# Performance work log

Measured on AMD Instinct MI355X. Metric: run time of the kernel, lower is better.

## Reference

```python
import jax, jax.numpy as jnp
import numpy as np

N = 50000
IN_DIM, HID, LAT = 128, 256, 64
E = 800000


def setup_inputs() -> dict:
    key = jax.random.key(0)
    ks = jax.random.split(key, 12)
    x = jax.random.normal(ks[0], (N, IN_DIM), dtype=jnp.float32)
    edge_index = jax.random.randint(ks[1], (2, E), 0, N, dtype=jnp.int64)
    edge_weight = jax.random.uniform(ks[2], (E,), dtype=jnp.float32)
    def w(k, i, o):
        return jax.random.normal(k, (i, o), dtype=jnp.float32) * 0.05
    return {
        "x": x, "edge_index": edge_index, "edge_weight": edge_weight,
        "W1": w(ks[3], IN_DIM, HID), "b1": jnp.zeros((HID,), jnp.float32),
        "W2": w(ks[4], HID, LAT),    "b2": jnp.zeros((LAT,), jnp.float32),
        "W3": w(ks[5], LAT, HID),    "b3": jnp.zeros((HID,), jnp.float32),
        "W4": w(ks[6], HID, IN_DIM), "b4": jnp.zeros((IN_DIM,), jnp.float32),
    }


def _gcn_norm(edge_index, edge_weight, n):
    # add self loops with weight 1 (PyG GCNConv default), symmetric normalization
    loop = jnp.arange(n, dtype=edge_index.dtype)
    row = jnp.concatenate([edge_index[0], loop])
    col = jnp.concatenate([edge_index[1], loop])
    ew = jnp.concatenate([edge_weight, jnp.ones((n,), edge_weight.dtype)])
    deg = jax.ops.segment_sum(ew, col, num_segments=n)  # [N]
    dinv = jnp.where(deg > 0, jax.lax.rsqrt(deg), 0.0)
    norm = dinv[row] * ew * dinv[col]                   # [E+N]
    return row, col, norm


def _gcn_conv(x, row, col, norm, W, b, n):
    h = x @ W                                           # [N, out]
    msg = h[row] * norm[:, None]                        # gather + scale [E+N, out]
    out = jax.ops.segment_sum(msg, col, num_segments=n) # scatter-add
    return out + b


def reference(x, edge_index, edge_weight, W1, b1, W2, b2, W3, b3, W4, b4):
    n = x.shape[0]
    row, col, norm = _gcn_norm(edge_index, edge_weight, n)
    # encode (dropout is identity in eval mode)
    h = jax.nn.relu(_gcn_conv(x, row, col, norm, W1, b1, n))
    z = _gcn_conv(h, row, col, norm, W2, b2, n)
    # decode
    h = jax.nn.relu(_gcn_conv(z, row, col, norm, W3, b3, n))
    x_recon = _gcn_conv(h, row, col, norm, W4, b4, n)
    return x_recon
```

## Files before the change

### kernel.cpp

```cpp
#include <hip/hip_runtime.h>
#include <hip/hip_fp16.h>

#define IN_DIM 128
#define HID    256
#define LAT    64

typedef __attribute__((ext_vector_type(8))) short bf16x8;
typedef __attribute__((ext_vector_type(4))) float f32x4;

__device__ __forceinline__ short f2bf(float f) {
    union { float f; unsigned u; } v; v.f = f;
    unsigned r = v.u + 0x7fffu + ((v.u >> 16) & 1u);
    return (short)(r >> 16);
}
__device__ __forceinline__ float bf2f(short s) {
    union { unsigned u; float f; } v; v.u = ((unsigned)(unsigned short)s) << 16;
    return v.f;
}

__device__ __forceinline__ void storeP(__half* p, float v) { *p = __float2half(v); }
__device__ __forceinline__ void storeP(float*  p, float v) { *p = v; }


#define FIXSCALE 1048576.0f

__global__ void k_init(unsigned long long* __restrict__ packed, int n) {
    int i = blockIdx.x * 256 + threadIdx.x;
    if (i < n) packed[i] = (unsigned long long)(1u << 20);
}

__global__ void k_edge_acc(const int* __restrict__ ei, const float* __restrict__ ew,
                           unsigned long long* __restrict__ packed,
                           int* __restrict__ rank, int E) {
    int e = blockIdx.x * 256 + threadIdx.x;
    if (e < E) {
        int c = ei[E + e];
        unsigned fx = (unsigned)lrintf(ew[e] * FIXSCALE);
        unsigned long long old =
            atomicAdd(&packed[c], ((unsigned long long)1 << 40) | (unsigned long long)fx);
        rank[e] = (int)(old >> 40);
    }
}

__global__ void k_derive(const unsigned long long* __restrict__ packed,
                         float* __restrict__ dinv, int* __restrict__ counts, int n) {
    int i = blockIdx.x * 256 + threadIdx.x;
    if (i < n) {
        unsigned long long p = packed[i];
        float deg = (float)(p & (((unsigned long long)1 << 40) - 1)) * (1.0f / FIXSCALE);
        dinv[i]   = rsqrtf(deg);
        counts[i] = (int)(p >> 40);
    }
}

__global__ __launch_bounds__(1024) void k_blocksum(const int* __restrict__ counts,
                                                   int* __restrict__ bsum, int n) {
    __shared__ int ws[16];
    const int t = threadIdx.x, lane = t & 63, wv = t >> 6;
    int i = blockIdx.x * 1024 + t;
    int v = (i < n) ? counts[i] : 0;
    #pragma unroll
    for (int d = 1; d < 64; d <<= 1) v += __shfl_xor(v, d);
    if (lane == 0) ws[wv] = v;
    __syncthreads();
    if (wv == 0 && lane < 16) {
        int x = ws[lane];
        #pragma unroll
        for (int d = 1; d < 16; d <<= 1) x += __shfl_xor(x, d, 16);
        if (lane == 0) bsum[blockIdx.x] = x;
    }
}

__global__ void k_scan_bsums(int* __restrict__ bsum, int nb,
                             int* __restrict__ offsets, int n) {
    int lane = threadIdx.x;
    int v = (lane < nb) ? bsum[lane] : 0;
    #pragma unroll
    for (int d = 1; d < 64; d <<= 1) {
        int u = __shfl_up(v, d);
        if (lane >= d) v += u;
    }
    if (lane < nb) bsum[lane] = v;
    if (lane == nb - 1) offsets[n] = v;
}

__global__ __launch_bounds__(1024) void k_scan_apply(const int* __restrict__ counts,
                                                     const int* __restrict__ bsum,
                                                     int* __restrict__ offsets, int n) {
    __shared__ int ws[16];
    const int t = threadIdx.x, lane = t & 63, wv = t >> 6;
    int i = blockIdx.x * 1024 + t;
    int v = (i < n) ? counts[i] : 0;
    int s = v;
    #pragma unroll
    for (int d = 1; d < 64; d <<= 1) {
        int u = __shfl_up(s, d);
        if (lane >= d) s += u;
    }
    if (lane == 63) ws[wv] = s;
    __syncthreads();
    if (wv == 0 && lane < 16) {
        int x = ws[lane];
        #pragma unroll
        for (int d = 1; d < 16; d <<= 1) {
            int u = __shfl_up(x, d, 16);
            if (lane >= d) x += u;
        }
        ws[lane] = x;
    }
    __syncthreads();
    int base = (blockIdx.x ? bsum[blockIdx.x - 1] : 0) + (wv ? ws[wv - 1] : 0);
    if (i < n) offsets[i] = base + s - v;
}

__global__ void k_fill(const int* __restrict__ ei, const float* __restrict__ ew,
                       const float* __restrict__ dinv, const int* __restrict__ offsets,
                       const int* __restrict__ rank,
                       int* __restrict__ csr_row, float* __restrict__ csr_norm, int E) {
    int e = blockIdx.x * 256 + threadIdx.x;
    if (e < E) {
        int r = ei[e];
        int c = ei[E + e];
        int pos = offsets[c] + rank[e];
        csr_row[pos]  = r;
        csr_norm[pos] = dinv[r] * ew[e] * dinv[c];
    }
}

template <int BN, typename PT>
__global__ __launch_bounds__(256) void gemm_mfma(const float* __restrict__ A,
                                                 const float* __restrict__ W,
                                                 PT* __restrict__ P,
                                                 int M, int K, int F) {
    constexpr int WC = BN / 32;
    __shared__ alignas(16) short Ahi[128][40];
    __shared__ alignas(16) short Alo[128][40];
    __shared__ alignas(16) short Whi[BN][40];
    __shared__ alignas(16) short Wlo[BN][40];

    const int bm  = blockIdx.x * 128;
    const int bn  = blockIdx.y * BN;
    const int tid = threadIdx.x;
    const int wv  = tid >> 6;
    const int wy  = wv >> 1;
    const int wx  = wv & 1;
    const int lane = tid & 63;
    const int frow = lane & 15;
    const int fk   = (lane >> 4) * 8;

    const int wc_ = tid % BN;
    const int kg  = tid / BN;
    constexpr int KC = 32 * BN / 256;

    f32x4 acc[4][WC];
    #pragma unroll
    for (int i = 0; i < 4; ++i)
        #pragma unroll
        for (int j = 0; j < WC; ++j)
            acc[i][j] = (f32x4){0.f, 0.f, 0.f, 0.f};

    for (int k0 = 0; k0 < K; k0 += 32) {
        if (k0) __syncthreads();
        #pragma unroll
        for (int it = 0; it < 4; ++it) {
            int l   = tid + it * 256;
            int row = l >> 3;
            int k4  = l & 7;
            int gr  = bm + row;
            float4 v = make_float4(0.f, 0.f, 0.f, 0.f);
            if (gr < M) v = *(const float4*)&A[(size_t)gr * K + k0 + k4 * 4];
            float vv[4] = {v.x, v.y, v.z, v.w};
            short h[4], lo[4];
            #pragma unroll
            for (int j = 0; j < 4; ++j) {
                h[j]  = f2bf(vv[j]);
                lo[j] = f2bf(vv[j] - bf2f(h[j]));
            }
            *(short4*)&Ahi[row][k4 * 4] = make_short4(h[0], h[1], h[2], h[3]);
            *(short4*)&Alo[row][k4 * 4] = make_short4(lo[0], lo[1], lo[2], lo[3]);
        }
        #pragma unroll
        for (int kk = 0; kk < KC; kk += 4) {
            short h[4], lo[4];
            #pragma unroll
            for (int j = 0; j < 4; ++j) {
                float w = W[(size_t)(k0 + kg * KC + kk + j) * F + bn + wc_];
                h[j]  = f2bf(w);
                lo[j] = f2bf(w - bf2f(h[j]));
            }
            *(short4*)&Whi[wc_][kg * KC + kk] = make_short4(h[0], h[1], h[2], h[3]);
            *(short4*)&Wlo[wc_][kg * KC + kk] = make_short4(lo[0], lo[1], lo[2], lo[3]);
        }
        __syncthreads();
        bf16x8 ah[4], al[4], wh[WC], wl[WC];
        #pragma unroll
        for (int ar = 0; ar < 4; ++ar) {
            ah[ar] = *(const bf16x8*)&Ahi[wy * 64 + ar * 16 + frow][fk];
            al[ar] = *(const bf16x8*)&Alo[wy * 64 + ar * 16 + frow][fk];
        }
        #pragma unroll
        for (int wc = 0; wc < WC; ++wc) {
            wh[wc] = *(const bf16x8*)&Whi[wx * (BN / 2) + wc * 16 + frow][fk];
            wl[wc] = *(const bf16x8*)&Wlo[wx * (BN / 2) + wc * 16 + frow][fk];
        }
        #pragma unroll
        for (int ar = 0; ar < 4; ++ar)
            #pragma unroll
            for (int wc = 0; wc < WC; ++wc) {
                acc[ar][wc] = __builtin_amdgcn_mfma_f32_16x16x32_bf16(ah[ar], wh[wc], acc[ar][wc], 0, 0, 0);
                acc[ar][wc] = __builtin_amdgcn_mfma_f32_16x16x32_bf16(ah[ar], wl[wc], acc[ar][wc], 0, 0, 0);
                acc[ar][wc] = __builtin_amdgcn_mfma_f32_16x16x32_bf16(al[ar], wh[wc], acc[ar][wc], 0, 0, 0);
            }
    }
    #pragma unroll
    for (int ar = 0; ar < 4; ++ar)
        #pragma unroll
        for (int r = 0; r < 4; ++r) {
            int row = bm + wy * 64 + ar * 16 + (lane >> 4) * 4 + r;
            if (row >= M) continue;
            #pragma unroll
            for (int wc = 0; wc < WC; ++wc) {
                int col = bn + wx * (BN / 2) + wc * 16 + (lane & 15);
                storeP(&P[(size_t)row * F + col], acc[ar][wc][r]);
            }
        }
}


template <int VEC>
__device__ __forceinline__ void pload(float* d, const __half* s) {
    if constexpr (VEC == 4) {
        union { short4 s4; __half h[4]; } u;
        u.s4 = *(const short4*)s;
        #pragma unroll
        for (int j = 0; j < 4; ++j) d[j] = __half2float(u.h[j]);
    } else if constexpr (VEC == 2) {
        union { short2 s2; __half h[2]; } u;
        u.s2 = *(const short2*)s;
        d[0] = __half2float(u.h[0]); d[1] = __half2float(u.h[1]);
    } else {
        d[0] = __half2float(*s);
    }
}
template <int VEC>
__device__ __forceinline__ void pload(float* d, const float* s) {
    if constexpr (VEC == 4) { float4 v = *(const float4*)s; d[0]=v.x; d[1]=v.y; d[2]=v.z; d[3]=v.w; }
    else if constexpr (VEC == 2) { float2 v = *(const float2*)s; d[0]=v.x; d[1]=v.y; }
    else { d[0] = *s; }
}
template <int VEC>
__device__ __forceinline__ void fstore(float* d, const float* s) {
    if constexpr (VEC == 4) { *(float4*)d = make_float4(s[0], s[1], s[2], s[3]); }
    else if constexpr (VEC == 2) { *(float2*)d = make_float2(s[0], s[1]); }
    else { *d = s[0]; }
}

template <int VEC, bool RELU, typename PT>
__global__ __launch_bounds__(256) void agg_kernel(
    const PT* __restrict__ pre, const float* __restrict__ bias,
    const int* __restrict__ offsets, const int* __restrict__ csr_row,
    const float* __restrict__ csr_norm, const float* __restrict__ dinv,
    float* __restrict__ out, int n) {
    constexpr int F = VEC * 64;
    const int wave = threadIdx.x >> 6;
    const int lane = threadIdx.x & 63;
    const int c = blockIdx.x * 4 + wave;
    if (c >= n) return;
    const float di = dinv[c];
    const float sn = di * di;
    float acc[VEC], t0[VEC], t1[VEC], t2[VEC], t3[VEC], bv[VEC];
    pload<VEC>(acc, pre + (size_t)c * F + lane * VEC);
    #pragma unroll
    for (int v = 0; v < VEC; ++v) acc[v] *= sn;
    const int beg = offsets[c], end = offsets[c + 1];
    int j = beg;
    for (; j + 3 < end; j += 4) {
        int   r0 = csr_row[j],      r1 = csr_row[j + 1];
        int   r2 = csr_row[j + 2],  r3 = csr_row[j + 3];
        float w0 = csr_norm[j],     w1 = csr_norm[j + 1];
        float w2 = csr_norm[j + 2], w3 = csr_norm[j + 3];
        pload<VEC>(t0, pre + (size_t)r0 * F + lane * VEC);
        pload<VEC>(t1, pre + (size_t)r1 * F + lane * VEC);
        pload<VEC>(t2, pre + (size_t)r2 * F + lane * VEC);
        pload<VEC>(t3, pre + (size_t)r3 * F + lane * VEC);
        #pragma unroll
        for (int v = 0; v < VEC; ++v) acc[v] = fmaf(w0, t0[v], acc[v]);
        #pragma unroll
        for (int v = 0; v < VEC; ++v) acc[v] = fmaf(w1, t1[v], acc[v]);
        #pragma unroll
        for (int v = 0; v < VEC; ++v) acc[v] = fmaf(w2, t2[v], acc[v]);
        #pragma unroll
        for (int v = 0; v < VEC; ++v) acc[v] = fmaf(w3, t3[v], acc[v]);
    }
    for (; j < end; ++j) {
        int r0 = csr_row[j]; float w0 = csr_norm[j];
        pload<VEC>(t0, pre + (size_t)r0 * F + lane * VEC);
        #pragma unroll
        for (int v = 0; v < VEC; ++v) acc[v] = fmaf(w0, t0[v], acc[v]);
    }
    pload<VEC>(bv, bias + lane * VEC);
    #pragma unroll
    for (int v = 0; v < VEC; ++v) {
        float o = acc[v] + bv[v];
        if (RELU) o = fmaxf(o, 0.f);
        acc[v] = o;
    }
    fstore<VEC>(out + (size_t)c * F + lane * VEC, acc);
}


extern "C" void kernel_launch(void* const* d_in, const int* in_sizes, int n_in,
                              void* d_out, int out_size, void* d_ws, size_t ws_size,
                              hipStream_t stream) {
    const float* x  = (const float*)d_in[0];
    const int*   ei = (const int*)  d_in[1];
    const float* ew = (const float*)d_in[2];
    const float* W1 = (const float*)d_in[3];
    const float* b1 = (const float*)d_in[4];
    const float* W2 = (const float*)d_in[5];
    const float* b2 = (const float*)d_in[6];
    const float* W3 = (const float*)d_in[7];
    const float* b3 = (const float*)d_in[8];
    const float* W4 = (const float*)d_in[9];
    const float* b4 = (const float*)d_in[10];

    const int N = in_sizes[0] / IN_DIM;
    const int E = in_sizes[2];

    char* p = (char*)d_ws;
    auto alloc = [&](size_t bytes) -> void* {
        void* r = (void*)p;
        p += (bytes + 255) & ~(size_t)255;
        return r;
    };
    unsigned long long* packed = (unsigned long long*)alloc((size_t)N * 8);
    float*  dinv     = (float*)alloc((size_t)N * 4);
    int*    counts   = (int*)  alloc((size_t)N * 4);
    int*    offsets  = (int*)  alloc((size_t)(N + 1) * 4);
    int*    bsum     = (int*)  alloc((size_t)64 * 4);
    int*    rank     = (int*)  alloc((size_t)E * 4);
    int*    csr_row  = (int*)  alloc((size_t)E * 4);
    float*  csr_norm = (float*)alloc((size_t)E * 4);
    __half* bufP     = (__half*)alloc((size_t)N * HID * 2);
    float*  bufH     = (float*) alloc((size_t)N * HID * 4);
    float*  bufZ     = (float*) alloc((size_t)N * LAT * 4);
    float*  bufP32   = (float*)bufP;

    const int gN  = (N + 255) / 256;
    const int gE  = (E + 255) / 256;
    const int nbS = (N + 1023) / 1024;
    const int nbM = (N + 127) / 128;
    const int nodeBlocks = (N + 3) / 4;

    k_init      <<<gN, 256, 0, stream>>>(packed, N);
    k_edge_acc  <<<gE, 256, 0, stream>>>(ei, ew, packed, rank, E);
    k_derive    <<<gN, 256, 0, stream>>>(packed, dinv, counts, N);
    k_blocksum  <<<nbS, 1024, 0, stream>>>(counts, bsum, N);
    k_scan_bsums<<<1, 64, 0, stream>>>(bsum, nbS, offsets, N);
    k_scan_apply<<<nbS, 1024, 0, stream>>>(counts, bsum, offsets, N);
    k_fill      <<<gE, 256, 0, stream>>>(ei, ew, dinv, offsets, rank, csr_row, csr_norm, E);

    gemm_mfma<128, __half><<<dim3(nbM, HID / 128), 256, 0, stream>>>(x, W1, bufP, N, IN_DIM, HID);
    agg_kernel<4, true, __half><<<nodeBlocks, 256, 0, stream>>>(bufP, b1, offsets, csr_row, csr_norm, dinv, bufH, N);

    gemm_mfma<64, __half><<<dim3(nbM, LAT / 64), 256, 0, stream>>>(bufH, W2, bufP, N, HID, LAT);
    agg_kernel<1, false, __half><<<nodeBlocks, 256, 0, stream>>>(bufP, b2, offsets, csr_row, csr_norm, dinv, bufZ, N);

    gemm_mfma<128, __half><<<dim3(nbM, HID / 128), 256, 0, stream>>>(bufZ, W3, bufP, N, LAT, HID);
    agg_kernel<4, true, __half><<<nodeBlocks, 256, 0, stream>>>(bufP, b3, offsets, csr_row, csr_norm, dinv, bufH, N);

    gemm_mfma<128, float><<<dim3(nbM, IN_DIM / 128), 256, 0, stream>>>(bufH, W4, bufP32, N, HID, IN_DIM);
    agg_kernel<2, false, float><<<nodeBlocks, 256, 0, stream>>>(bufP32, b4, offsets, csr_row, csr_norm, dinv, (float*)d_out, N);
}
```

Baseline: 480.9 us.

## Reorder GCN layers to aggregate at narrower width and fuse bias+ReLU into GEMM

For layers 1 and 3, the aggregation now runs before the matrix multiply, using associativity (A·X)·W. The gather therefore runs at 128 or 64 features instead of 256, and the bias+ReLU is applied in the GEMM epilogue. Edge row indices and norms are packed into one int2 CSR array so each edge needs a single load, and the input x is cast to fp16 first to halve gather traffic. The cost is an extra cast kernel and fp16 rounding of x and z, which could change accuracy.

```diff
diff --git a/kernel.cpp b/kernel.cpp
--- a/kernel.cpp
+++ b/kernel.cpp
@@ -116,20 +116,35 @@
 __global__ void k_fill(const int* __restrict__ ei, const float* __restrict__ ew,
                        const float* __restrict__ dinv, const int* __restrict__ offsets,
                        const int* __restrict__ rank,
-                       int* __restrict__ csr_row, float* __restrict__ csr_norm, int E) {
+                       int2* __restrict__ csr, int E) {
     int e = blockIdx.x * 256 + threadIdx.x;
     if (e < E) {
         int r = ei[e];
         int c = ei[E + e];
         int pos = offsets[c] + rank[e];
-        csr_row[pos]  = r;
-        csr_norm[pos] = dinv[r] * ew[e] * dinv[c];
-    }
-}
-
-template <int BN, typename PT>
+        float nm = dinv[r] * ew[e] * dinv[c];
+        csr[pos] = make_int2(r, __float_as_int(nm));
+    }
+}
+
+__global__ void k_cast(const float* __restrict__ x, __half* __restrict__ xh, int total) {
+    int idx = (blockIdx.x * 256 + threadIdx.x) * 8;
+    if (idx < total) {
+        float4 a = *(const float4*)&x[idx];
+        float4 b = *(const float4*)&x[idx + 4];
+        short4 s0 = make_short4(__half_as_short(__float2half(a.x)), __half_as_short(__float2half(a.y)),
+                                __half_as_short(__float2half(a.z)), __half_as_short(__float2half(a.w)));
+        short4 s1 = make_short4(__half_as_short(__float2half(b.x)), __half_as_short(__float2half(b.y)),
+                                __half_as_short(__float2half(b.z)), __half_as_short(__float2half(b.w)));
+        *(short4*)&xh[idx]     = s0;
+        *(short4*)&xh[idx + 4] = s1;
+    }
+}
+
+template <int BN, typename PT, bool EPI>
 __global__ __launch_bounds__(256) void gemm_mfma(const float* __restrict__ A,
                                                  const float* __restrict__ W,
+                                                 const float* __restrict__ bias,
                                                  PT* __restrict__ P,
                                                  int M, int K, int F) {
     constexpr int WC = BN / 32;
@@ -221,7 +236,9 @@
             #pragma unroll
             for (int wc = 0; wc < WC; ++wc) {
                 int col = bn + wx * (BN / 2) + wc * 16 + (lane & 15);
-                storeP(&P[(size_t)row * F + col], acc[ar][wc][r]);
+                float o = acc[ar][wc][r];
+                if (EPI) o = fmaxf(o + bias[col], 0.f);
+                storeP(&P[(size_t)row * F + col], o);
             }
         }
 }
@@ -249,18 +266,28 @@
     else { d[0] = *s; }
 }
 template <int VEC>
-__device__ __forceinline__ void fstore(float* d, const float* s) {
+__device__ __forceinline__ void pstore(__half* d, const float* s) {
+    if constexpr (VEC == 4) {
+        *(short4*)d = make_short4(__half_as_short(__float2half(s[0])), __half_as_short(__float2half(s[1])),
+                                  __half_as_short(__float2half(s[2])), __half_as_short(__float2half(s[3])));
+    } else if constexpr (VEC == 2) {
+        *(short2*)d = make_short2(__half_as_short(__float2half(s[0])), __half_as_short(__float2half(s[1])));
+    } else {
+        *d = __float2half(s[0]);
+    }
+}
+template <int VEC>
+__device__ __forceinline__ void pstore(float* d, const float* s) {
     if constexpr (VEC == 4) { *(float4*)d = make_float4(s[0], s[1], s[2], s[3]); }
     else if constexpr (VEC == 2) { *(float2*)d = make_float2(s[0], s[1]); }
     else { *d = s[0]; }
 }
 
-template <int VEC, bool RELU, typename PT>
+template <int VEC, bool HASB, typename TIN, typename TOUT>
 __global__ __launch_bounds__(256) void agg_kernel(
-    const PT* __restrict__ pre, const float* __restrict__ bias,
-    const int* __restrict__ offsets, const int* __restrict__ csr_row,
-    const float* __restrict__ csr_norm, const float* __restrict__ dinv,
-    float* __restrict__ out, int n) {
+    const TIN* __restrict__ pre, const float* __restrict__ bias,
+    const int* __restrict__ offsets, const int2* __restrict__ csr,
+    const float* __restrict__ dinv, TOUT* __restrict__ out, int n) {
     constexpr int F = VEC * 64;
     const int wave = threadIdx.x >> 6;
     const int lane = threadIdx.x & 63;
@@ -268,44 +295,41 @@
     if (c >= n) return;
     const float di = dinv[c];
     const float sn = di * di;
-    float acc[VEC], t0[VEC], t1[VEC], t2[VEC], t3[VEC], bv[VEC];
+    float acc[VEC], t0[VEC], t1[VEC], t2[VEC], t3[VEC];
     pload<VEC>(acc, pre + (size_t)c * F + lane * VEC);
     #pragma unroll
     for (int v = 0; v < VEC; ++v) acc[v] *= sn;
     const int beg = offsets[c], end = offsets[c + 1];
     int j = beg;
     for (; j + 3 < end; j += 4) {
-        int   r0 = csr_row[j],      r1 = csr_row[j + 1];
-        int   r2 = csr_row[j + 2],  r3 = csr_row[j + 3];
-        float w0 = csr_norm[j],     w1 = csr_norm[j + 1];
-        float w2 = csr_norm[j + 2], w3 = csr_norm[j + 3];
-        pload<VEC>(t0, pre + (size_t)r0 * F + lane * VEC);
-        pload<VEC>(t1, pre + (size_t)r1 * F + lane * VEC);
-        pload<VEC>(t2, pre + (size_t)r2 * F + lane * VEC);
-        pload<VEC>(t3, pre + (size_t)r3 * F + lane * VEC);
-        #pragma unroll
-        for (int v = 0; v < VEC; ++v) acc[v] = fmaf(w0, t0[v], acc[v]);
-        #pragma unroll
-        for (int v = 0; v < VEC; ++v) acc[v] = fmaf(w1, t1[v], acc[v]);
-        #pragma unroll
-        for (int v = 0; v < VEC; ++v) acc[v] = fmaf(w2, t2[v], acc[v]);
-        #pragma unroll
-        for (int v = 0; v < VEC; ++v) acc[v] = fmaf(w3, t3[v], acc[v]);
+        int2 e0 = csr[j],     e1 = csr[j + 1];
+        int2 e2 = csr[j + 2], e3 = csr[j + 3];
+        pload<VEC>(t0, pre + (size_t)e0.x * F + lane * VEC);
+        pload<VEC>(t1, pre + (size_t)e1.x * F + lane * VEC);
+        pload<VEC>(t2, pre + (size_t)e2.x * F + lane * VEC);
+        pload<VEC>(t3, pre + (size_t)e3.x * F + lane * VEC);
+        #pragma unroll
+        for (int v = 0; v < VEC; ++v) acc[v] = fmaf(__int_as_float(e0.y), t0[v], acc[v]);
+        #pragma unroll
+        for (int v = 0; v < VEC; ++v) acc[v] = fmaf(__int_as_float(e1.y), t1[v], acc[v]);
+        #pragma unroll
+        for (int v = 0; v < VEC; ++v) acc[v] = fmaf(__int_as_float(e2.y), t2[v], acc[v]);
+        #pragma unroll
+        for (int v = 0; v < VEC; ++v) acc[v] = fmaf(__int_as_float(e3.y), t3[v], acc[v]);
     }
     for (; j < end; ++j) {
-        int r0 = csr_row[j]; float w0 = csr_norm[j];
-        pload<VEC>(t0, pre + (size_t)r0 * F + lane * VEC);
-        #pragma unroll
-        for (int v = 0; v < VEC; ++v) acc[v] = fmaf(w0, t0[v], acc[v]);
-    }
-    pload<VEC>(bv, bias + lane * VEC);
-    #pragma unroll
-    for (int v = 0; v < VEC; ++v) {
-        float o = acc[v] + bv[v];
-        if (RELU) o = fmaxf(o, 0.f);
-        acc[v] = o;
-    }
-    fstore<VEC>(out + (size_t)c * F + lane * VEC, acc);
+        int2 e0 = csr[j];
+        pload<VEC>(t0, pre + (size_t)e0.x * F + lane * VEC);
+        #pragma unroll
+        for (int v = 0; v < VEC; ++v) acc[v] = fmaf(__int_as_float(e0.y), t0[v], acc[v]);
+    }
+    if (HASB) {
+        float bv[VEC];
+        pload<VEC>(bv, bias + lane * VEC);
+        #pragma unroll
+        for (int v = 0; v < VEC; ++v) acc[v] += bv[v];
+    }
+    pstore<VEC>(out + (size_t)c * F + lane * VEC, acc);
 }
 
 
@@ -339,18 +363,21 @@
     int*    offsets  = (int*)  alloc((size_t)(N + 1) * 4);
     int*    bsum     = (int*)  alloc((size_t)64 * 4);
     int*    rank     = (int*)  alloc((size_t)E * 4);
-    int*    csr_row  = (int*)  alloc((size_t)E * 4);
-    float*  csr_norm = (float*)alloc((size_t)E * 4);
-    __half* bufP     = (__half*)alloc((size_t)N * HID * 2);
-    float*  bufH     = (float*) alloc((size_t)N * HID * 4);
-    float*  bufZ     = (float*) alloc((size_t)N * LAT * 4);
-    float*  bufP32   = (float*)bufP;
+    int2*   csr      = (int2*) alloc((size_t)E * 8);
+    __half* xh       = (__half*)alloc((size_t)N * IN_DIM * 2);
+    float*  ha       = (float*) alloc((size_t)N * IN_DIM * 4);
+    float*  h        = (float*) alloc((size_t)N * HID * 4);
+    __half* P2       = (__half*)alloc((size_t)N * LAT * 2);
+    __half* zh       = (__half*)alloc((size_t)N * LAT * 2);
+    float*  za       = (float*)xh;
+    float*  P4       = ha;
 
     const int gN  = (N + 255) / 256;
     const int gE  = (E + 255) / 256;
     const int nbS = (N + 1023) / 1024;
     const int nbM = (N + 127) / 128;
     const int nodeBlocks = (N + 3) / 4;
+    const int castBlocks = (N * IN_DIM / 8 + 255) / 256;
 
     k_init      <<<gN, 256, 0, stream>>>(packed, N);
     k_edge_acc  <<<gE, 256, 0, stream>>>(ei, ew, packed, rank, E);
@@ -358,17 +385,18 @@
     k_blocksum  <<<nbS, 1024, 0, stream>>>(counts, bsum, N);
     k_scan_bsums<<<1, 64, 0, stream>>>(bsum, nbS, offsets, N);
     k_scan_apply<<<nbS, 1024, 0, stream>>>(counts, bsum, offsets, N);
-    k_fill      <<<gE, 256, 0, stream>>>(ei, ew, dinv, offsets, rank, csr_row, csr_norm, E);
-
-    gemm_mfma<128, __half><<<dim3(nbM, HID / 128), 256, 0, stream>>>(x, W1, bufP, N, IN_DIM, HID);
-    agg_kernel<4, true, __half><<<nodeBlocks, 256, 0, stream>>>(bufP, b1, offsets, csr_row, csr_norm, dinv, bufH, N);
-
-    gemm_mfma<64, __half><<<dim3(nbM, LAT / 64), 256, 0, stream>>>(bufH, W2, bufP, N, HID, LAT);
-    agg_kernel<1, false, __half><<<nodeBlocks, 256, 0, stream>>>(bufP, b2, offsets, csr_row, csr_norm, dinv, bufZ, N);
-
-    gemm_mfma<128, __half><<<dim3(nbM, HID / 128), 256, 0, stream>>>(bufZ, W3, bufP, N, LAT, HID);
-    agg_kernel<4, true, __half><<<nodeBlocks, 256, 0, stream>>>(bufP, b3, offsets, csr_row, csr_norm, dinv, bufH, N);
-
-    gemm_mfma<128, float><<<dim3(nbM, IN_DIM / 128), 256, 0, stream>>>(bufH, W4, bufP32, N, HID, IN_DIM);
-    agg_kernel<2, false, float><<<nodeBlocks, 256, 0, stream>>>(bufP32, b4, offsets, csr_row, csr_norm, dinv, (float*)d_out, N);
-}
+    k_fill      <<<gE, 256, 0, stream>>>(ei, ew, dinv, offsets, rank, csr, E);
+    k_cast      <<<castBlocks, 256, 0, stream>>>(x, xh, N * IN_DIM);
+
+    agg_kernel<2, false, __half, float><<<nodeBlocks, 256, 0, stream>>>(xh, nullptr, offsets, csr, dinv, ha, N);
+    gemm_mfma<128, float, true><<<dim3(nbM, HID / 128), 256, 0, stream>>>(ha, W1, b1, h, N, IN_DIM, HID);
+
+    gemm_mfma<64, __half, false><<<dim3(nbM, LAT / 64), 256, 0, stream>>>(h, W2, nullptr, P2, N, HID, LAT);
+    agg_kernel<1, true, __half, __half><<<nodeBlocks, 256, 0, stream>>>(P2, b2, offsets, csr, dinv, zh, N);
+
+    agg_kernel<1, false, __half, float><<<nodeBlocks, 256, 0, stream>>>(zh, nullptr, offsets, csr, dinv, za, N);
+    gemm_mfma<128, float, true><<<dim3(nbM, HID / 128), 256, 0, stream>>>(za, W3, b3, h, N, LAT, HID);
+
+    gemm_mfma<128, float, false><<<dim3(nbM, IN_DIM / 128), 256, 0, stream>>>(h, W4, nullptr, P4, N, HID, IN_DIM);
+    agg_kernel<2, true, float, float><<<nodeBlocks, 256, 0, stream>>>(P4, b4, offsets, csr, dinv, (float*)d_out, N);
+}
```

Result: faster. 441.0 us (-8.3%).
